# Optimization experiments

Hardware: AMD Instinct MI355X
Metric: run time of the kernel (lower is better)

Reference implementation:

```python
import jax, jax.numpy as jnp
import numpy as np

NV = [12544, 6272, 3136, 1568, 784]  # vertex counts, fine -> coarse
SPIRAL = 9


def _grid_sample(im, grid):
    """Faithful port of the hand-rolled bilinear_grid_sample, align_corners=True.
    im: (n, c, h, w); grid: (n, gh, gw, 2) in [-1, 1]. Returns (n, c, gh*gw)."""
    n, c, h, w = im.shape
    gx = grid[..., 0].reshape(n, -1)
    gy = grid[..., 1].reshape(n, -1)
    x = (gx + 1) / 2 * (w - 1)
    y = (gy + 1) / 2 * (h - 1)
    x0 = jnp.floor(x); y0 = jnp.floor(y)
    x1 = x0 + 1; y1 = y0 + 1
    wa = (x1 - x) * (y1 - y)
    wb = (x1 - x) * (y - y0)
    wc = (x - x0) * (y1 - y)
    wd = (x - x0) * (y - y0)
    imp = jnp.pad(im, ((0, 0), (0, 0), (1, 1), (1, 1)))  # explicit zero pad as in source
    ph, pw = h + 2, w + 2
    x0i = jnp.clip(x0.astype(jnp.int32) + 1, 0, pw - 1)
    x1i = jnp.clip(x1.astype(jnp.int32) + 1, 0, pw - 1)
    y0i = jnp.clip(y0.astype(jnp.int32) + 1, 0, ph - 1)
    y1i = jnp.clip(y1.astype(jnp.int32) + 1, 0, ph - 1)
    impf = imp.reshape(n, c, -1)

    def gat(xi, yi):
        idx = xi + yi * pw  # (n, P)
        return jnp.take_along_axis(impf, idx[:, None, :], axis=2)  # (n, c, P)

    Ia = gat(x0i, y0i); Ib = gat(x0i, y1i); Ic = gat(x1i, y0i); Id = gat(x1i, y1i)
    return Ia * wa[:, None] + Ib * wb[:, None] + Ic * wc[:, None] + Id * wd[:, None]


def _pool(x, col, val):
    """Mesh up-pooling: gather columns, weight, and 3-way sum per output vertex.
    With row = repeat(arange(n_out), 3) the row_map built in __init__ is exactly
    arange(3*n_out).reshape(n_out, 3), so the three gathers reduce to reshape+sum."""
    out = x[:, col, :] * val[None, :, None]  # (B, 3*n_out, C)
    n_out = val.shape[0] // 3
    return out.reshape(x.shape[0], n_out, 3, x.shape[2]).sum(axis=2)


def _dsconv(x, idx, dw, pw):
    """Depthwise-separable spiral conv: gather spiral neighborhood, depthwise
    conv over spiral dim (per-channel), then 1x1 pointwise projection."""
    gsp = x[:, idx, :]                        # (B, N, S, Cin)
    y = jnp.einsum('bnsc,cs->bnc', gsp, dw)   # depthwise over spiral
    return y @ pw                             # (B, N, Cout)


def setup_inputs() -> dict:
    key = jax.random.key(0)
    ks = jax.random.split(key, 32)
    d = {}
    d['uv'] = jax.random.uniform(ks[0], (16, 64, 2), jnp.float32)
    d['feat'] = jax.random.normal(ks[1], (16, 256, 4, 4), jnp.float32)
    d['upsample'] = jax.random.normal(ks[2], (NV[4], 64), jnp.float32) * 0.01
    chs = [(256, 256), (256, 256), (256, 128), (128, 64)]
    for i, (ci, co) in enumerate(chs):
        d['dw%d' % i] = jax.random.normal(ks[3 + 2 * i], (ci, SPIRAL), jnp.float32) * (1.0 / SPIRAL)
        d['pw%d' % i] = jax.random.normal(ks[4 + 2 * i], (ci, co), jnp.float32) * (ci ** -0.5)
    d['dw_head'] = jax.random.normal(ks[11], (64, SPIRAL), jnp.float32) * (1.0 / SPIRAL)
    d['pw_head'] = jax.random.normal(ks[12], (64, 3), jnp.float32) * (64 ** -0.5)
    for j in range(4):
        n_out, n_in = NV[j], NV[j + 1]
        d['sp_idx_%d' % j] = jax.random.randint(ks[13 + j], (NV[j], SPIRAL), 0, NV[j], dtype=jnp.int32)
        d['up_col_%d' % j] = jax.random.randint(ks[17 + j], (3 * n_out,), 0, n_in, dtype=jnp.int32)
        d['up_val_%d' % j] = jax.random.uniform(ks[21 + j], (3 * n_out,), jnp.float32)
    return d


def reference(uv, feat, upsample, dw0, pw0, dw1, pw1, dw2, pw2, dw3, pw3, dw_head, pw_head,
              up_val_0, up_val_1, up_val_2, up_val_3,
              sp_idx_0, sp_idx_1, sp_idx_2, sp_idx_3,
              up_col_0, up_col_1, up_col_2, up_col_3):
    g = jnp.clip((uv - 0.5) * 2.0, -1.0, 1.0)[:, :, None, :]  # (B, P, 1, 2)
    x = _grid_sample(feat, g)            # (B, 256, P)
    x = x.transpose(0, 2, 1)             # (B, P, 256)
    x = jnp.einsum('vp,bpc->bvc', upsample, x)  # (B, 784, 256) coarse mesh feats
    specs = [(up_col_3, up_val_3, sp_idx_3, dw0, pw0),
             (up_col_2, up_val_2, sp_idx_2, dw1, pw1),
             (up_col_1, up_val_1, sp_idx_1, dw2, pw2),
             (up_col_0, up_val_0, sp_idx_0, dw3, pw3)]
    for col, val, idx, dw, pw in specs:
        x = _pool(x, col, val)
        x = jax.nn.relu(_dsconv(x, idx, dw, pw))
    return _dsconv(x, sp_idx_0, dw_head, pw_head)  # (B, 12544, 3)
```

## Files before the change

kernel.cpp:

```cpp
#include <hip/hip_runtime.h>


typedef _Float16 half8 __attribute__((ext_vector_type(8)));
typedef float    f32x4 __attribute__((ext_vector_type(4)));

__device__ __forceinline__ float4 ld4(const float* p) { return *(const float4*)p; }

__device__ __forceinline__ float lo16f(unsigned u) {
  _Float16 h; unsigned short s = (unsigned short)(u & 0xffffu);
  __builtin_memcpy(&h, &s, 2); return (float)h;
}
__device__ __forceinline__ float hi16f(unsigned u) {
  _Float16 h; unsigned short s = (unsigned short)(u >> 16);
  __builtin_memcpy(&h, &s, 2); return (float)h;
}
__device__ __forceinline__ float h2f(unsigned short s) {
  _Float16 h; __builtin_memcpy(&h, &s, 2); return (float)h;
}
__device__ __forceinline__ unsigned short hbits(float v) {
  _Float16 h = (_Float16)v; unsigned short u; __builtin_memcpy(&u, &h, 2); return u;
}
__device__ __forceinline__ unsigned pk2h(float a, float b) {
  return (unsigned)hbits(a) | ((unsigned)hbits(b) << 16);
}
__device__ __forceinline__ void split2h(float v, unsigned short& h, unsigned short& l) {
  _Float16 hf = (_Float16)v;
  float hif = (float)hf;
  _Float16 lf = (_Float16)((v - hif) * 2048.0f);
  __builtin_memcpy(&h, &hf, 2); __builtin_memcpy(&l, &lf, 2);
}
__device__ __forceinline__ void gload_lds16(const unsigned short* g, unsigned short* l) {
  __builtin_amdgcn_global_load_lds(
      (const __attribute__((address_space(1))) unsigned int*)g,
      (__attribute__((address_space(3))) unsigned int*)l, 16, 0, 0);
}

__global__ __launch_bounds__(256) void k_prep_all(
    const float* __restrict__ pw0, const float* __restrict__ pw1,
    const float* __restrict__ pw2, const float* __restrict__ pw3,
    const float* __restrict__ dwh, const float* __restrict__ pwh,
    const float* __restrict__ dw0, const float* __restrict__ dw1,
    const float* __restrict__ dw2, const float* __restrict__ dw3,
    unsigned short* __restrict__ dstPw, unsigned short* __restrict__ dstHead,
    float* __restrict__ dstDw)
{
  const int blk = blockIdx.x, t = threadIdx.x;
  if (blk < 672) {
    const int b = blk;
    const float* src; int ci_sh, co, f, off;
    if (b < 256)      { src = pw0; ci_sh = 8; co = 256; f = b*256 + t;       off = 0; }
    else if (b < 512) { src = pw1; ci_sh = 8; co = 256; f = (b-256)*256 + t; off = 65536; }
    else if (b < 640) { src = pw2; ci_sh = 8; co = 128; f = (b-512)*256 + t; off = 131072; }
    else              { src = pw3; ci_sh = 7; co = 64;  f = (b-640)*256 + t; off = 163840; }
    const int n = f >> ci_sh, k = f & ((1 << ci_sh) - 1);
    float v = src[(size_t)k*co + n];
    unsigned short h, l; split2h(v, h, l);
    dstPw[off + f]          = h;
    dstPw[172032 + off + f] = l;
  } else if (blk < 680) {
    const int i = (blk - 672)*256 + t;
    const int n = i >> 6, c = i & 63;
    float v = 0.f;
    if (n < 27) v = dwh[c*9 + n/3] * pwh[c*3 + n%3];
    unsigned short h, l; split2h(v, h, l);
    dstHead[i] = h; dstHead[2048 + i] = l;
  } else {
    const int i = (blk - 680)*256 + t;
    if (i >= 8064) return;
    const float* src; int rel, C, off;
    if (i < 2304)      { src = dw0; rel = i;        C = 256; off = 0; }
    else if (i < 4608) { src = dw1; rel = i - 2304; C = 256; off = 2304; }
    else if (i < 6912) { src = dw2; rel = i - 4608; C = 256; off = 4608; }
    else               { src = dw3; rel = i - 6912; C = 128; off = 6912; }
    const int s = rel / C, c = rel % C;
    dstDw[off + rel] = src[c*9 + s];
  }
}

__global__ __launch_bounds__(256) void k_samp(
    const float* __restrict__ uv, const float* __restrict__ feat,
    unsigned short* __restrict__ xs)
{
  __shared__ float feat_l[256][17];
  const int tid = threadIdx.x;
  const int b   = blockIdx.x;

  const float* fr = feat + ((size_t)b*256 + tid)*16;
  #pragma unroll
  for (int i = 0; i < 16; i += 4) {
    float4 f = ld4(fr + i);
    feat_l[tid][i+0] = f.x; feat_l[tid][i+1] = f.y;
    feat_l[tid][i+2] = f.z; feat_l[tid][i+3] = f.w;
  }
  #pragma unroll 4
  for (int p = 0; p < 64; ++p) {
    float gx = uv[((size_t)b*64 + p)*2 + 0];
    float gy = uv[((size_t)b*64 + p)*2 + 1];
    gx = fminf(fmaxf((gx - 0.5f)*2.f, -1.f), 1.f);
    gy = fminf(fmaxf((gy - 0.5f)*2.f, -1.f), 1.f);
    float x = (gx + 1.f)*0.5f*3.f;
    float y = (gy + 1.f)*0.5f*3.f;
    float fx = floorf(x), fy = floorf(y);
    int ix0 = (int)fx, iy0 = (int)fy;
    float wx = x - fx, wy = y - fy;
    int ix1 = ix0 + 1 > 3 ? 3 : ix0 + 1;
    int iy1 = iy0 + 1 > 3 ? 3 : iy0 + 1;
    float v00 = feat_l[tid][iy0*4+ix0];
    float v01 = feat_l[tid][iy0*4+ix1];
    float v10 = feat_l[tid][iy1*4+ix0];
    float v11 = feat_l[tid][iy1*4+ix1];
    float xv = (1.f-wy)*((1.f-wx)*v00 + wx*v01) + wy*((1.f-wx)*v10 + wx*v11);
    xs[((size_t)b*64 + p)*256 + tid] = hbits(xv);
  }
}

__global__ __launch_bounds__(256) void k_up(
    const unsigned short* __restrict__ xs, const float* __restrict__ up,
    unsigned short* __restrict__ x0)
{
  const int tid = threadIdx.x;
  const int b   = blockIdx.y;
  const int v0  = blockIdx.x * 16;

  float acc[16];
  #pragma unroll
  for (int i = 0; i < 16; ++i) acc[i] = 0.f;

  #pragma unroll 8
  for (int p = 0; p < 64; ++p) {
    const float xv = h2f(xs[((size_t)b*64 + p)*256 + tid]);
    #pragma unroll
    for (int i = 0; i < 16; ++i)
      acc[i] += up[(size_t)(v0+i)*64 + p] * xv;
  }
  #pragma unroll
  for (int i = 0; i < 16; ++i)
    x0[((size_t)b*784 + v0 + i)*256 + tid] = hbits(acc[i]);
}

template<int C>
__global__ __launch_bounds__(256) void k_pool(
    const unsigned short* __restrict__ x, const int* __restrict__ col,
    const float* __restrict__ val, unsigned short* __restrict__ out,
    int Vin, int Vout)
{
  constexpr int KGc = C/8;
  constexpr int UPB = 2*KGc;
  const int bp = blockIdx.x & 7;
  const int v0 = (blockIdx.x >> 3) * 8;
  const int t  = threadIdx.x;

  #pragma unroll
  for (int i = 0; i < (8*UPB)/256; ++i) {
    const int id = t + i*256;
    const int vl = id / UPB;
    const int rem = id - vl*UPB;
    const int bl = rem / KGc;
    const int kg = rem - bl*KGc;
    const int v  = v0 + vl;
    const int b  = 2*bp + bl;
    const int c0 = col[3*v+0], c1 = col[3*v+1], c2 = col[3*v+2];
    const float w0 = val[3*v+0], w1 = val[3*v+1], w2 = val[3*v+2];
    const uint4 A = *(const uint4*)(x + ((size_t)b*Vin + c0)*C + 8*kg);
    const uint4 B = *(const uint4*)(x + ((size_t)b*Vin + c1)*C + 8*kg);
    const uint4 Cv= *(const uint4*)(x + ((size_t)b*Vin + c2)*C + 8*kg);
    uint4 R;
    R.x = pk2h(w0*lo16f(A.x)+w1*lo16f(B.x)+w2*lo16f(Cv.x),
               w0*hi16f(A.x)+w1*hi16f(B.x)+w2*hi16f(Cv.x));
    R.y = pk2h(w0*lo16f(A.y)+w1*lo16f(B.y)+w2*lo16f(Cv.y),
               w0*hi16f(A.y)+w1*hi16f(B.y)+w2*hi16f(Cv.y));
    R.z = pk2h(w0*lo16f(A.z)+w1*lo16f(B.z)+w2*lo16f(Cv.z),
               w0*hi16f(A.z)+w1*hi16f(B.z)+w2*hi16f(Cv.z));
    R.w = pk2h(w0*lo16f(A.w)+w1*lo16f(B.w)+w2*lo16f(Cv.w),
               w0*hi16f(A.w)+w1*hi16f(B.w)+w2*hi16f(Cv.w));
    *(uint4*)(out + ((size_t)b*Vout + v)*C + 8*kg) = R;
  }
}

template<int CI>
__global__ __launch_bounds__(256) void k_dw(
    const unsigned short* __restrict__ pin, const int* __restrict__ idx,
    const float* __restrict__ dwT, unsigned short* __restrict__ aout,
    int Vin, int VG)
{
  constexpr int KG    = CI/8;
  constexpr int SLOTS = 256/KG;
  constexpr int VPB   = 2*SLOTS;

  const int t     = threadIdx.x;
  const int xcd   = blockIdx.x & 7;
  const int i     = blockIdx.x >> 3;
  const int phase = (i >= VG) ? 1 : 0;
  const int vg    = i - phase*VG;
  const int b     = xcd + 8*phase;
  const int kg    = t & (KG - 1);
  const int slot  = t / KG;
  const int va    = vg*VPB + slot;
  const int vb2   = va + SLOTS;

  const unsigned short* base = pin + (size_t)b*Vin*CI + 8*kg;
  float y0[8], y1[8];
  #pragma unroll
  for (int j = 0; j < 8; ++j) { y0[j] = 0.f; y1[j] = 0.f; }

  #pragma unroll
  for (int s = 0; s < 9; ++s) {
    const float4 wa = *(const float4*)(dwT + s*CI + 8*kg);
    const float4 wb = *(const float4*)(dwT + s*CI + 8*kg + 4);
    const uint4 g0 = *(const uint4*)(base + (size_t)idx[va *9 + s]*CI);
    const uint4 g1 = *(const uint4*)(base + (size_t)idx[vb2*9 + s]*CI);
    y0[0] += wa.x*lo16f(g0.x); y0[1] += wa.y*hi16f(g0.x);
    y0[2] += wa.z*lo16f(g0.y); y0[3] += wa.w*hi16f(g0.y);
    y0[4] += wb.x*lo16f(g0.z); y0[5] += wb.y*hi16f(g0.z);
    y0[6] += wb.z*lo16f(g0.w); y0[7] += wb.w*hi16f(g0.w);
    y1[0] += wa.x*lo16f(g1.x); y1[1] += wa.y*hi16f(g1.x);
    y1[2] += wa.z*lo16f(g1.y); y1[3] += wa.w*hi16f(g1.y);
    y1[4] += wb.x*lo16f(g1.z); y1[5] += wb.y*hi16f(g1.z);
    y1[6] += wb.z*lo16f(g1.w); y1[7] += wb.w*hi16f(g1.w);
  }
  uint4 p0, p1;
  p0.x = pk2h(y0[0], y0[1]); p0.y = pk2h(y0[2], y0[3]);
  p0.z = pk2h(y0[4], y0[5]); p0.w = pk2h(y0[6], y0[7]);
  p1.x = pk2h(y1[0], y1[1]); p1.y = pk2h(y1[2], y1[3]);
  p1.z = pk2h(y1[4], y1[5]); p1.w = pk2h(y1[6], y1[7]);
  *(uint4*)(aout + (size_t)(va *16 + b)*CI + 8*kg) = p0;
  *(uint4*)(aout + (size_t)(vb2*16 + b)*CI + 8*kg) = p1;
}

template<int CI, int COT, int NTW, int NSLICE, bool RELU>
__global__ __launch_bounds__(256) void k_gemm(
    const unsigned short* __restrict__ A,
    const unsigned short* __restrict__ bhp, const unsigned short* __restrict__ blp,
    unsigned short* __restrict__ out, int Vout, int T)
{
  constexpr int CHUNKS = CI/32;
  constexpr int NCOL   = NTW*64;
  constexpr int OROW   = NCOL + 8;
  constexpr int ABYTES = 64*CI*2;
  constexpr int SLOTS  = ABYTES/16;
  constexpr int AUS    = SLOTS*8;
  constexpr int NB     = (NSLICE == 1) ? 2 : 1;

  __shared__ __align__(16) unsigned short a_l[NB*AUS];
  __shared__ __align__(16) unsigned short epi[(NSLICE==2) ? 64*OROW : 1];

  const int t = threadIdx.x;
  const int w = t >> 6, l = t & 15, q = (t >> 4) & 3;
  const int lane6 = t & 63;
  const int tix0 = blockIdx.x * T;
  const int coB  = blockIdx.y * NCOL * NSLICE;

  auto stage = [&](int tix, int sel) {
    const size_t m0 = (size_t)tix * 64;
    unsigned short* dst = a_l + (size_t)sel*AUS;
    #pragma unroll
    for (int r = 0; r < SLOTS/256; ++r) {
      const int s    = t + r*256;
      const int c    = s >> 8;
      const int mt   = (s >> 6) & 3;
      const int ql   = s & 63;
      const int m    = mt*16 + (ql & 15);
      const int koff = c*32 + (ql >> 4)*8;
      gload_lds16(A + (m0 + m)*CI + koff, dst + (size_t)s*8);
    }
  };

  if constexpr (NSLICE == 1) {
    stage(tix0, 0);
    __syncthreads();
    for (int j = 0; j < T; ++j) {
      const int tix = tix0 + j;
      const int sel = j & 1;
      if (j + 1 < T) stage(tix + 1, sel ^ 1);

      const unsigned short* ab = a_l + (size_t)sel*AUS;
      f32x4 ah[4][NTW], ax[4][NTW];
      #pragma unroll
      for (int mt = 0; mt < 4; ++mt)
        #pragma unroll
        for (int n = 0; n < NTW; ++n)
          #pragma unroll
          for (int r = 0; r < 4; ++r) { ah[mt][n][r] = 0.f; ax[mt][n][r] = 0.f; }

      #pragma unroll
      for (int c = 0; c < CHUNKS; ++c) {
        const int k0 = c*32 + q*8;
        half8 fa[4], fbh[NTW], fbl[NTW];
        #pragma unroll
        for (int mt = 0; mt < 4; ++mt)
          fa[mt] = *(const half8*)(ab + (size_t)(c*256 + mt*64 + lane6)*8);
        #pragma unroll
        for (int n = 0; n < NTW; ++n) {
          const size_t boff = (size_t)(coB + (w*NTW + n)*16 + l)*CI + k0;
          fbh[n] = *(const half8*)(bhp + boff);
          fbl[n] = *(const half8*)(blp + boff);
        }
        #pragma unroll
        for (int mt = 0; mt < 4; ++mt)
          #pragma unroll
          for (int n = 0; n < NTW; ++n) {
            ah[mt][n] = __builtin_amdgcn_mfma_f32_16x16x32_f16(fa[mt], fbh[n], ah[mt][n], 0, 0, 0);
            ax[mt][n] = __builtin_amdgcn_mfma_f32_16x16x32_f16(fa[mt], fbl[n], ax[mt][n], 0, 0, 0);
          }
      }

      __syncthreads();
      unsigned short (*ot)[OROW] = (unsigned short (*)[OROW])(a_l + (size_t)sel*AUS);
      #pragma unroll
      for (int mt = 0; mt < 4; ++mt)
        #pragma unroll
        for (int n = 0; n < NTW; ++n) {
          const int colg = (w*NTW + n)*16 + l;
          #pragma unroll
          for (int r = 0; r < 4; ++r) {
            const int row = mt*16 + q*4 + r;
            float v = ah[mt][n][r] + ax[mt][n][r] * (1.0f/2048.0f);
            if (RELU) v = fmaxf(v, 0.f);
            ot[row][colg] = hbits(v);
          }
        }
      __syncthreads();
      constexpr int PR = NCOL/8;
      const size_t m0 = (size_t)tix * 64;
      #pragma unroll
      for (int i = 0; i < (64*PR)/256; ++i) {
        const int item = t + i*256;
        const int r  = item / PR;
        const int cp = (item % PR)*8;
        const size_t m = m0 + r;
        const int v = (int)(m >> 4), b = (int)(m & 15);
        *(uint4*)(out + ((size_t)b*Vout + v)*COT + coB + cp) = *(const uint4*)&ot[r][cp];
      }
      __syncthreads();
    }
  } else {
    unsigned short (*ot)[OROW] = (unsigned short (*)[OROW])&epi[0];
    for (int j = 0; j < T; ++j) {
      const int tix = tix0 + j;
      stage(tix, 0);
      __syncthreads();
      #pragma unroll
      for (int sl = 0; sl < 2; ++sl) {
        const int co0 = coB + sl*NCOL;
        f32x4 ah[4][NTW], ax[4][NTW];
        #pragma unroll
        for (int mt = 0; mt < 4; ++mt)
          #pragma unroll
          for (int n = 0; n < NTW; ++n)
            #pragma unroll
            for (int r = 0; r < 4; ++r) { ah[mt][n][r] = 0.f; ax[mt][n][r] = 0.f; }

        #pragma unroll
        for (int c = 0; c < CHUNKS; ++c) {
          const int k0 = c*32 + q*8;
          half8 fa[4], fbh[NTW], fbl[NTW];
          #pragma unroll
          for (int mt = 0; mt < 4; ++mt)
            fa[mt] = *(const half8*)(a_l + (size_t)(c*256 + mt*64 + lane6)*8);
          #pragma unroll
          for (int n = 0; n < NTW; ++n) {
            const size_t boff = (size_t)(co0 + (w*NTW + n)*16 + l)*CI + k0;
            fbh[n] = *(const half8*)(bhp + boff);
            fbl[n] = *(const half8*)(blp + boff);
          }
          #pragma unroll
          for (int mt = 0; mt < 4; ++mt)
            #pragma unroll
            for (int n = 0; n < NTW; ++n) {
              ah[mt][n] = __builtin_amdgcn_mfma_f32_16x16x32_f16(fa[mt], fbh[n], ah[mt][n], 0, 0, 0);
              ax[mt][n] = __builtin_amdgcn_mfma_f32_16x16x32_f16(fa[mt], fbl[n], ax[mt][n], 0, 0, 0);
            }
        }

        __syncthreads();
        #pragma unroll
        for (int mt = 0; mt < 4; ++mt)
          #pragma unroll
          for (int n = 0; n < NTW; ++n) {
            const int colg = (w*NTW + n)*16 + l;
            #pragma unroll
            for (int r = 0; r < 4; ++r) {
              const int row = mt*16 + q*4 + r;
              float v = ah[mt][n][r] + ax[mt][n][r] * (1.0f/2048.0f);
              if (RELU) v = fmaxf(v, 0.f);
              ot[row][colg] = hbits(v);
            }
          }
        __syncthreads();
        constexpr int PR = NCOL/8;
        const size_t m0 = (size_t)tix * 64;
        #pragma unroll
        for (int i = 0; i < (64*PR)/256; ++i) {
          const int item = t + i*256;
          const int r  = item / PR;
          const int cp = (item % PR)*8;
          const size_t m = m0 + r;
          const int v = (int)(m >> 4), b = (int)(m & 15);
          *(uint4*)(out + ((size_t)b*Vout + v)*COT + co0 + cp) = *(const uint4*)&ot[r][cp];
        }
      }
      __syncthreads();
    }
  }
}

__global__ __launch_bounds__(256) void k_headz(
    const unsigned short* __restrict__ A,
    const unsigned short* __restrict__ bhT, const unsigned short* __restrict__ blT,
    float* __restrict__ z)
{
  __shared__ float zt[4][32][16];

  const int t = threadIdx.x;
  const size_t m0 = (size_t)blockIdx.x * 64;
  const int w = t >> 6, l = t & 15, q = (t >> 4) & 3;

  f32x4 acch[2], accl[2];
  #pragma unroll
  for (int n = 0; n < 2; ++n)
    #pragma unroll
    for (int r = 0; r < 4; ++r) { acch[n][r] = 0.f; accl[n][r] = 0.f; }

  const size_t m = m0 + w*16 + l;
  const size_t arow = ((m & 15)*12544 + (m >> 4))*64;
  #pragma unroll
  for (int c = 0; c < 2; ++c) {
    const int k0 = c*32 + q*8;
    half8 fa = *(const half8*)(A + arow + k0);
    #pragma unroll
    for (int n = 0; n < 2; ++n) {
      half8 fbh = *(const half8*)(bhT + (size_t)(n*16 + l)*64 + k0);
      half8 fbl = *(const half8*)(blT + (size_t)(n*16 + l)*64 + k0);
      acch[n] = __builtin_amdgcn_mfma_f32_16x16x32_f16(fa, fbh, acch[n], 0, 0, 0);
      accl[n] = __builtin_amdgcn_mfma_f32_16x16x32_f16(fa, fbl, accl[n], 0, 0, 0);
    }
  }

  #pragma unroll
  for (int n = 0; n < 2; ++n)
    #pragma unroll
    for (int r = 0; r < 4; ++r)
      zt[w][n*16 + l][q*4 + r] = acch[n][r] + accl[n][r] * (1.0f/2048.0f);
  __syncthreads();

  const size_t u0 = m0 >> 4;
  #pragma unroll
  for (int i = 0; i < 7; ++i) {
    const int item = t + i*256;
    if (item < 1728) {
      const int ul  = item / 432;
      const int rem = item - ul*432;
      const int s   = rem / 48;
      const int bj  = rem - s*48;
      const int b   = bj / 3;
      const int j   = bj - b*3;
      z[(u0 + ul)*432 + rem] = zt[ul][s*3 + j][b];
    }
  }
}

__global__ __launch_bounds__(256) void k_head2(
    const float* __restrict__ z, const int* __restrict__ idx,
    float* __restrict__ out, int nvert)
{
  const int w    = threadIdx.x >> 6;
  const int lane = threadIdx.x & 63;
  const int v    = blockIdx.x*4 + w;
  if (lane < 48) {
    float acc = 0.f;
    #pragma unroll
    for (int s = 0; s < 9; ++s) {
      const int u = idx[v*9 + s];
      acc += z[(size_t)u*432 + s*48 + lane];
    }
    const int b = lane / 3, j = lane - b*3;
    out[((size_t)b*nvert + v)*3 + j] = acc;
  }
}

extern "C" void kernel_launch(void* const* d_in, const int* in_sizes, int n_in,
                              void* d_out, int out_size, void* d_ws, size_t ws_size,
                              hipStream_t stream)
{
  const float* uv   = (const float*)d_in[0];
  const float* feat = (const float*)d_in[1];
  const float* up   = (const float*)d_in[2];
  const float* dw0  = (const float*)d_in[3];
  const float* pw0  = (const float*)d_in[4];
  const float* dw1  = (const float*)d_in[5];
  const float* pw1  = (const float*)d_in[6];
  const float* dw2  = (const float*)d_in[7];
  const float* pw2  = (const float*)d_in[8];
  const float* dw3  = (const float*)d_in[9];
  const float* pw3  = (const float*)d_in[10];
  const float* dwh  = (const float*)d_in[11];
  const float* pwh  = (const float*)d_in[12];
  const int*   sp0  = (const int*)d_in[13];
  const int*   col0 = (const int*)d_in[14];
  const float* val0 = (const float*)d_in[15];
  const int*   sp1  = (const int*)d_in[16];
  const int*   col1 = (const int*)d_in[17];
  const float* val1 = (const float*)d_in[18];
  const int*   sp2  = (const int*)d_in[19];
  const int*   col2 = (const int*)d_in[20];
  const float* val2 = (const float*)d_in[21];
  const int*   sp3  = (const int*)d_in[22];
  const int*   col3 = (const int*)d_in[23];
  const float* val3 = (const float*)d_in[24];

  unsigned short* bufA  = (unsigned short*)d_ws;
  unsigned short* bufB  = (unsigned short*)((char*)d_ws + 25690112);
  unsigned short* bufC  = (unsigned short*)((char*)d_ws + 77070336);
  unsigned short* pwT   = (unsigned short*)((char*)d_ws + 128450560);
  unsigned short* bhead = (unsigned short*)((char*)d_ws + 129138688);
  float*          dwT   = (float*)((char*)d_ws + 129155072);
  float*          zbuf  = (float*)((char*)d_ws + 129187328);
  unsigned short* xs    = (unsigned short*)((char*)d_ws + 150863360);
  float* outp = (float*)d_out;

  unsigned short* h0 = pwT;            unsigned short* L0 = pwT + 172032;
  unsigned short* h1 = pwT + 65536;    unsigned short* L1 = L0 + 65536;
  unsigned short* h2 = pwT + 131072;   unsigned short* L2 = L0 + 131072;
  unsigned short* h3 = pwT + 163840;   unsigned short* L3 = L0 + 163840;
  unsigned short* hh = bhead;          unsigned short* Lh = bhead + 2048;
  float* dwT0 = dwT;          float* dwT1 = dwT + 2304;
  float* dwT2 = dwT + 4608;   float* dwT3 = dwT + 6912;

  k_prep_all<<<712, 256, 0, stream>>>(pw0, pw1, pw2, pw3, dwh, pwh,
                                      dw0, dw1, dw2, dw3, pwT, bhead, dwT);
  k_samp<<<16, 256, 0, stream>>>(uv, feat, xs);
  k_up<<<dim3(49,16,1), 256, 0, stream>>>(xs, up, bufA);

  k_pool<256><<<1568, 256, 0, stream>>>(bufA, col3, val3, bufB, 784, 1568);
  k_dw<256><<<16*98, 256, 0, stream>>>(bufB, sp3, dwT0, bufC, 1568, 98);
  k_gemm<256,256,2,2,true><<<dim3(196,1), 256, 0, stream>>>(bufC, h0, L0, bufA, 1568, 2);

  k_pool<256><<<3136, 256, 0, stream>>>(bufA, col2, val2, bufB, 1568, 3136);
  k_dw<256><<<16*196, 256, 0, stream>>>(bufB, sp2, dwT1, bufC, 3136, 196);
  k_gemm<256,256,2,2,true><<<dim3(392,1), 256, 0, stream>>>(bufC, h1, L1, bufA, 3136, 2);

  k_pool<256><<<6272, 256, 0, stream>>>(bufA, col1, val1, bufB, 3136, 6272);
  k_dw<256><<<16*392, 256, 0, stream>>>(bufB, sp1, dwT2, bufC, 6272, 392);
  k_gemm<256,128,2,1,true><<<dim3(392,1), 256, 0, stream>>>(bufC, h2, L2, bufA, 6272, 4);

  k_pool<128><<<12544, 256, 0, stream>>>(bufA, col0, val0, bufB, 6272, 12544);
  k_dw<128><<<16*392, 256, 0, stream>>>(bufB, sp0, dwT3, bufC, 12544, 392);
  k_gemm<128,64,1,1,true><<<dim3(784,1), 256, 0, stream>>>(bufC, h3, L3, bufA, 12544, 4);

  k_headz<<<3136, 256, 0, stream>>>(bufA, hh, Lh, zbuf);
  k_head2<<<3136, 256, 0, stream>>>(zbuf, sp0, outp, 12544);
}
```

Before: 413.0 us.

## Fuse final pointwise GEMM with head projection to skip intermediate buffer

```diff
diff --git a/kernel.cpp b/kernel.cpp
--- a/kernel.cpp
+++ b/kernel.cpp
@@ -339,7 +339,7 @@
       const int tix = tix0 + j;
       stage(tix, 0);
       __syncthreads();
-      #pragma unroll
+      #pragma unroll 1
       for (int sl = 0; sl < 2; ++sl) {
         const int co0 = coB + sl*NCOL;
         f32x4 ah[4][NTW], ax[4][NTW];
@@ -404,58 +404,128 @@
   }
 }
 
-__global__ __launch_bounds__(256) void k_headz(
+__global__ __launch_bounds__(256) void k_gemm_head(
     const unsigned short* __restrict__ A,
+    const unsigned short* __restrict__ bhp, const unsigned short* __restrict__ blp,
     const unsigned short* __restrict__ bhT, const unsigned short* __restrict__ blT,
-    float* __restrict__ z)
-{
+    float* __restrict__ z, int T)
+{
+  constexpr int CI     = 128;
+  constexpr int CHUNKS = 4;
+  constexpr int OROW   = 80;
+  constexpr int ABYTES = 64*CI*2;
+  constexpr int SLOTS  = ABYTES/16;
+  constexpr int AUS    = SLOTS*8;
+
+  __shared__ __align__(16) unsigned short a_l[2*AUS];
   __shared__ float zt[4][32][16];
 
   const int t = threadIdx.x;
-  const size_t m0 = (size_t)blockIdx.x * 64;
   const int w = t >> 6, l = t & 15, q = (t >> 4) & 3;
-
-  f32x4 acch[2], accl[2];
-  #pragma unroll
-  for (int n = 0; n < 2; ++n)
-    #pragma unroll
-    for (int r = 0; r < 4; ++r) { acch[n][r] = 0.f; accl[n][r] = 0.f; }
-
-  const size_t m = m0 + w*16 + l;
-  const size_t arow = ((m & 15)*12544 + (m >> 4))*64;
-  #pragma unroll
-  for (int c = 0; c < 2; ++c) {
-    const int k0 = c*32 + q*8;
-    half8 fa = *(const half8*)(A + arow + k0);
-    #pragma unroll
-    for (int n = 0; n < 2; ++n) {
-      half8 fbh = *(const half8*)(bhT + (size_t)(n*16 + l)*64 + k0);
-      half8 fbl = *(const half8*)(blT + (size_t)(n*16 + l)*64 + k0);
-      acch[n] = __builtin_amdgcn_mfma_f32_16x16x32_f16(fa, fbh, acch[n], 0, 0, 0);
-      accl[n] = __builtin_amdgcn_mfma_f32_16x16x32_f16(fa, fbl, accl[n], 0, 0, 0);
-    }
-  }
-
-  #pragma unroll
-  for (int n = 0; n < 2; ++n)
-    #pragma unroll
-    for (int r = 0; r < 4; ++r)
-      zt[w][n*16 + l][q*4 + r] = acch[n][r] + accl[n][r] * (1.0f/2048.0f);
+  const int lane6 = t & 63;
+  const int tix0 = blockIdx.x * T;
+
+  auto stage = [&](int tix, int sel) {
+    const size_t m0 = (size_t)tix * 64;
+    unsigned short* dst = a_l + (size_t)sel*AUS;
+    #pragma unroll
+    for (int r = 0; r < SLOTS/256; ++r) {
+      const int s    = t + r*256;
+      const int c    = s >> 8;
+      const int mt   = (s >> 6) & 3;
+      const int ql   = s & 63;
+      const int m    = mt*16 + (ql & 15);
+      const int koff = c*32 + (ql >> 4)*8;
+      gload_lds16(A + (m0 + m)*CI + koff, dst + (size_t)s*8);
+    }
+  };
+
+  stage(tix0, 0);
   __syncthreads();
-
-  const size_t u0 = m0 >> 4;
-  #pragma unroll
-  for (int i = 0; i < 7; ++i) {
-    const int item = t + i*256;
-    if (item < 1728) {
-      const int ul  = item / 432;
-      const int rem = item - ul*432;
-      const int s   = rem / 48;
-      const int bj  = rem - s*48;
-      const int b   = bj / 3;
-      const int j   = bj - b*3;
-      z[(u0 + ul)*432 + rem] = zt[ul][s*3 + j][b];
-    }
+  for (int j = 0; j < T; ++j) {
+    const int tix = tix0 + j;
+    const int sel = j & 1;
+    if (j + 1 < T) stage(tix + 1, sel ^ 1);
+
+    const unsigned short* ab = a_l + (size_t)sel*AUS;
+    f32x4 ah[4], ax[4];
+    #pragma unroll
+    for (int mt = 0; mt < 4; ++mt)
+      #pragma unroll
+      for (int r = 0; r < 4; ++r) { ah[mt][r] = 0.f; ax[mt][r] = 0.f; }
+
+    #pragma unroll
+    for (int c = 0; c < CHUNKS; ++c) {
+      const int k0 = c*32 + q*8;
+      half8 fa[4];
+      #pragma unroll
+      for (int mt = 0; mt < 4; ++mt)
+        fa[mt] = *(const half8*)(ab + (size_t)(c*256 + mt*64 + lane6)*8);
+      const size_t boff = (size_t)(w*16 + l)*CI + k0;
+      half8 fbh = *(const half8*)(bhp + boff);
+      half8 fbl = *(const half8*)(blp + boff);
+      #pragma unroll
+      for (int mt = 0; mt < 4; ++mt) {
+        ah[mt] = __builtin_amdgcn_mfma_f32_16x16x32_f16(fa[mt], fbh, ah[mt], 0, 0, 0);
+        ax[mt] = __builtin_amdgcn_mfma_f32_16x16x32_f16(fa[mt], fbl, ax[mt], 0, 0, 0);
+      }
+    }
+
+    __syncthreads();
+    unsigned short (*ot)[OROW] = (unsigned short (*)[OROW])(a_l + (size_t)sel*AUS);
+    #pragma unroll
+    for (int mt = 0; mt < 4; ++mt) {
+      const int colg = w*16 + l;
+      #pragma unroll
+      for (int r = 0; r < 4; ++r) {
+        const int row = mt*16 + q*4 + r;
+        float v = ah[mt][r] + ax[mt][r] * (1.0f/2048.0f);
+        ot[row][colg] = hbits(fmaxf(v, 0.f));
+      }
+    }
+    __syncthreads();
+
+    {
+      f32x4 acch[2], accl[2];
+      #pragma unroll
+      for (int n = 0; n < 2; ++n)
+        #pragma unroll
+        for (int r = 0; r < 4; ++r) { acch[n][r] = 0.f; accl[n][r] = 0.f; }
+      #pragma unroll
+      for (int c = 0; c < 2; ++c) {
+        const int k0 = c*32 + q*8;
+        half8 fa = *(const half8*)&ot[w*16 + l][k0];
+        #pragma unroll
+        for (int n = 0; n < 2; ++n) {
+          half8 fbh = *(const half8*)(bhT + (size_t)(n*16 + l)*64 + k0);
+          half8 fbl = *(const half8*)(blT + (size_t)(n*16 + l)*64 + k0);
+          acch[n] = __builtin_amdgcn_mfma_f32_16x16x32_f16(fa, fbh, acch[n], 0, 0, 0);
+          accl[n] = __builtin_amdgcn_mfma_f32_16x16x32_f16(fa, fbl, accl[n], 0, 0, 0);
+        }
+      }
+      #pragma unroll
+      for (int n = 0; n < 2; ++n)
+        #pragma unroll
+        for (int r = 0; r < 4; ++r)
+          zt[w][n*16 + l][q*4 + r] = acch[n][r] + accl[n][r] * (1.0f/2048.0f);
+    }
+    __syncthreads();
+
+    const size_t u0 = (size_t)tix * 4;
+    #pragma unroll
+    for (int i = 0; i < 7; ++i) {
+      const int item = t + i*256;
+      if (item < 1728) {
+        const int ul  = item / 432;
+        const int rem = item - ul*432;
+        const int s   = rem / 48;
+        const int bj  = rem - s*48;
+        const int b   = bj / 3;
+        const int jj  = bj - b*3;
+        z[(u0 + ul)*432 + rem] = zt[ul][s*3 + jj][b];
+      }
+    }
+    __syncthreads();
   }
 }
 
@@ -545,8 +615,7 @@
 
   k_pool<128><<<12544, 256, 0, stream>>>(bufA, col0, val0, bufB, 6272, 12544);
   k_dw<128><<<16*392, 256, 0, stream>>>(bufB, sp0, dwT3, bufC, 12544, 392);
-  k_gemm<128,64,1,1,true><<<dim3(784,1), 256, 0, stream>>>(bufC, h3, L3, bufA, 12544, 4);
-
-  k_headz<<<3136, 256, 0, stream>>>(bufA, hh, Lh, zbuf);
+  k_gemm_head<<<dim3(784,1), 256, 0, stream>>>(bufC, h3, L3, hh, Lh, zbuf, 4);
+
   k_head2<<<3136, 256, 0, stream>>>(zbuf, sp0, outp, 12544);
 }
```

Measured after the change: 402.9 us (median of 2 runs). 2.4% less time.
